# Performance work log

Hardware: AMD Instinct MI355X
Metric: run time of the kernel (lower is better)

## Reference

```python
import jax, jax.numpy as jnp
import numpy as np

DIM = 384
NUM_HEADS = 12
HEAD_DIM = DIM // NUM_HEADS  # 32
SCALE = HEAD_DIM ** -0.5
B, N = 4, 2048


def setup_inputs() -> dict:
    key = jax.random.key(0)
    k0, k1, k2, k3 = jax.random.split(key, 4)
    x = jax.random.normal(k0, (B, N, DIM), dtype=jnp.float32)
    # nn.Linear(dim, 3*dim, bias=False): y = x @ W_qkv, W_qkv is [C, 3C]
    W_qkv = jax.random.normal(k1, (DIM, 3 * DIM), dtype=jnp.float32) * (DIM ** -0.5)
    # nn.Linear(dim, dim): y = x @ W_proj + b_proj, W_proj is [C, C]
    W_proj = jax.random.normal(k2, (DIM, DIM), dtype=jnp.float32) * (DIM ** -0.5)
    b_proj = jax.random.normal(k3, (DIM,), dtype=jnp.float32) * 0.01
    return {"x": x, "W_qkv": W_qkv, "W_proj": W_proj, "b_proj": b_proj}


def reference(x, W_qkv, W_proj, b_proj):
    b, n, c = x.shape
    qkv = (x @ W_qkv).reshape(b, n, 3, NUM_HEADS, HEAD_DIM)
    qkv = jnp.transpose(qkv, (2, 0, 3, 1, 4))  # [3, B, H, N, hd]
    q, k, v = qkv[0], qkv[1], qkv[2]
    # full attention: softmax(q k^T * scale) v
    attn = jnp.einsum('bhqd,bhkd->bhqk', q, k) * SCALE  # [B,H,N,N]
    attn = jax.nn.softmax(attn, axis=-1)
    out = jnp.einsum('bhqk,bhkd->bhqd', attn, v)  # [B,H,N,hd]
    out = jnp.transpose(out, (0, 2, 1, 3)).reshape(b, n, c)
    return out @ W_proj + b_proj
```

## Files before the change

### kernel.cpp

```cpp
#include <hip/hip_runtime.h>

constexpr int BB  = 4;
constexpr int SEQ = 2048;
constexpr int CC  = 384;
constexpr int C3  = 1152;
constexpr int NH  = 12;
constexpr int HD  = 32;
constexpr float SCALE = 0.17677669529663689f;
constexpr float LOG2E = 1.4426950408889634f;
constexpr size_t KV_BYTES = (size_t)2 * BB * NH * SEQ * HD * 2;
constexpr size_t WT_BYTES = ((size_t)C3 * CC + (size_t)CC * CC) * 2;
constexpr size_t XB_BYTES = (size_t)BB * SEQ * CC * 2;

typedef __attribute__((ext_vector_type(8))) short short8_t;
typedef __attribute__((ext_vector_type(4))) float floatx4;

#if __has_builtin(__builtin_amdgcn_exp2f)
#define EXP2F __builtin_amdgcn_exp2f
#else
#define EXP2F __builtin_exp2f
#endif

__device__ __forceinline__ unsigned short f2bf(float f) {
    unsigned int u = __builtin_bit_cast(unsigned int, f);
    u += 0x7fffu + ((u >> 16) & 1u);
    return (unsigned short)(u >> 16);
}
__device__ __forceinline__ unsigned int pk_rn(float lo, float hi) {
    return __builtin_amdgcn_perm(__builtin_bit_cast(unsigned int, hi) + 0x8000u,
                                 __builtin_bit_cast(unsigned int, lo) + 0x8000u,
                                 0x07060302u);
}
__device__ __forceinline__ short8_t pack8(float4 a, float4 b) {
    uint4 u;
    u.x = pk_rn(a.x, a.y); u.y = pk_rn(a.z, a.w);
    u.z = pk_rn(b.x, b.y); u.w = pk_rn(b.z, b.w);
    return __builtin_bit_cast(short8_t, u);
}

__global__ __launch_bounds__(256) void prep_kernel(
    const float* __restrict__ x, const float* __restrict__ wqkv,
    const float* __restrict__ wproj,
    unsigned short* __restrict__ wqkvT, unsigned short* __restrict__ wprojT,
    unsigned short* __restrict__ xb)
{
    const int bid = blockIdx.x;
    if (bid >= 144) {
        const size_t base = (size_t)(bid - 144) * 2048 + threadIdx.x * 8;
        const float4 a = *(const float4*)(x + base);
        const float4 b = *(const float4*)(x + base + 4);
        uint4 u;
        u.x = pk_rn(a.x, a.y); u.y = pk_rn(a.z, a.w);
        u.z = pk_rn(b.x, b.y); u.w = pk_rn(b.z, b.w);
        *(uint4*)(xb + base) = u;
        return;
    }
    __shared__ float ls[64][68];
    const float* src; unsigned short* dst; int SN, k0, n0;
    if (bid < 108) {
        src = wqkv; dst = wqkvT; SN = C3;
        k0 = (bid / 18) * 64; n0 = (bid % 18) * 64;
    } else {
        const int b2 = bid - 108;
        src = wproj; dst = wprojT; SN = CC;
        k0 = (b2 / 6) * 64; n0 = (b2 % 6) * 64;
    }
    const int t  = threadIdx.x;
    const int rr = t >> 4, cc4 = (t & 15) * 4;
#pragma unroll
    for (int p = 0; p < 4; ++p) {
        const int row = p * 16 + rr;
        const float4 v = *(const float4*)&src[(size_t)(k0 + row) * SN + n0 + cc4];
        ls[row][cc4] = v.x; ls[row][cc4 + 1] = v.y;
        ls[row][cc4 + 2] = v.z; ls[row][cc4 + 3] = v.w;
    }
    __syncthreads();
#pragma unroll
    for (int p = 0; p < 4; ++p) {
        const int nrow = p * 16 + rr;
        uint2 u;
        u.x = pk_rn(ls[cc4][nrow],     ls[cc4 + 1][nrow]);
        u.y = pk_rn(ls[cc4 + 2][nrow], ls[cc4 + 3][nrow]);
        *(uint2*)&dst[(size_t)(n0 + nrow) * CC + k0 + cc4] = u;
    }
}

template<bool XB>
__global__ __launch_bounds__(256) void qkv_fast_t(
    const float* __restrict__ x,
    const unsigned short* __restrict__ xb,
    const unsigned short* __restrict__ wT,
    float* __restrict__ dq,
    unsigned short* __restrict__ kv)
{
    __shared__ __align__(16) unsigned short As[2][128][40];
    __shared__ __align__(16) unsigned short Bs[2][128][40];

    const int mt   = blockIdx.x & 63;
    const int nb   = blockIdx.x >> 6;
    const int tid  = threadIdx.x;
    const int wid  = tid >> 6;
    const int lane = tid & 63;
    const int quad = lane >> 4;
    const int col  = lane & 15;
    const int wr   = wid >> 1, wc = wid & 1;
    const int m0 = mt * 128, n0 = nb * 128;

    const int arow = tid >> 1;
    const int aoff = (tid & 1) * 16;

    floatx4 acc[4][4];
#pragma unroll
    for (int i = 0; i < 4; ++i)
#pragma unroll
        for (int j = 0; j < 4; ++j) acc[i][j] = (floatx4){0.f, 0.f, 0.f, 0.f};

    const float*          xrow  = x  + (size_t)(m0 + arow) * CC + aoff;
    const unsigned short* xbrow = xb + (size_t)(m0 + arow) * CC + aoff;
    const unsigned short* wrow  = wT + (size_t)(n0 + arow) * CC + aoff;

    short8_t ast0, ast1, bst0, bst1;
    if (XB) {
        ast0 = *(const short8_t*)xbrow;
        ast1 = *(const short8_t*)(xbrow + 8);
    } else {
        ast0 = pack8(*(const float4*)xrow,       *(const float4*)(xrow + 4));
        ast1 = pack8(*(const float4*)(xrow + 8), *(const float4*)(xrow + 12));
    }
    bst0 = *(const short8_t*)wrow;
    bst1 = *(const short8_t*)(wrow + 8);
    *(short8_t*)&As[0][arow][aoff]     = ast0;
    *(short8_t*)&As[0][arow][aoff + 8] = ast1;
    *(short8_t*)&Bs[0][arow][aoff]     = bst0;
    *(short8_t*)&Bs[0][arow][aoff + 8] = bst1;

    for (int it = 0; it < CC / 32; ++it) {
        const int kn = (it + 1 < CC / 32) ? (it + 1) * 32 : 0;
        if (XB) {
            ast0 = *(const short8_t*)(xbrow + kn);
            ast1 = *(const short8_t*)(xbrow + kn + 8);
        } else {
            const float* xr = xrow + kn;
            ast0 = pack8(*(const float4*)xr,       *(const float4*)(xr + 4));
            ast1 = pack8(*(const float4*)(xr + 8), *(const float4*)(xr + 12));
        }
        bst0 = *(const short8_t*)(wrow + kn);
        bst1 = *(const short8_t*)(wrow + kn + 8);

        __syncthreads();
        const int p = it & 1;
        short8_t af[4], bf[4];
#pragma unroll
        for (int i = 0; i < 4; ++i)
            af[i] = *(const short8_t*)&As[p][wr * 64 + i * 16 + col][quad * 8];
#pragma unroll
        for (int j = 0; j < 4; ++j)
            bf[j] = *(const short8_t*)&Bs[p][wc * 64 + j * 16 + col][quad * 8];
#pragma unroll
        for (int j = 0; j < 4; ++j)
#pragma unroll
            for (int i = 0; i < 4; ++i)
                acc[i][j] = __builtin_amdgcn_mfma_f32_16x16x32_bf16(af[i], bf[j], acc[i][j], 0, 0, 0);

        *(short8_t*)&As[p ^ 1][arow][aoff]     = ast0;
        *(short8_t*)&As[p ^ 1][arow][aoff + 8] = ast1;
        *(short8_t*)&Bs[p ^ 1][arow][aoff]     = bst0;
        *(short8_t*)&Bs[p ^ 1][arow][aoff + 8] = bst1;
    }

    const int t = nb / 3;
#pragma unroll
    for (int i = 0; i < 4; ++i) {
        const int mg = m0 + wr * 64 + i * 16 + quad * 4;
        if (t == 0) {
#pragma unroll
            for (int j = 0; j < 4; ++j) {
                const int n = n0 + wc * 64 + j * 16 + col;
#pragma unroll
                for (int r = 0; r < 4; ++r)
                    dq[(size_t)(mg + r) * CC + n] = acc[i][j][r];
            }
        } else if (t == 1) {
            const int b = mg >> 11, s = mg & (SEQ - 1);
#pragma unroll
            for (int j = 0; j < 4; ++j) {
                const int rem = n0 - CC + wc * 64 + j * 16 + col;
                const int h = rem >> 5, d = rem & 31;
                unsigned short* kp = kv + ((size_t)(b * NH + h) * SEQ + s) * HD + d;
#pragma unroll
                for (int r = 0; r < 4; ++r)
                    kp[(size_t)r * HD] = f2bf(acc[i][j][r]);
            }
        } else {
            const int b = mg >> 11, s = mg & (SEQ - 1);
            unsigned short* vtb = kv + (size_t)BB * NH * SEQ * HD;
#pragma unroll
            for (int j = 0; j < 4; ++j) {
                const int rem = n0 - 2 * CC + wc * 64 + j * 16 + col;
                const int h = rem >> 5, d = rem & 31;
                uint2 u;
                u.x = pk_rn(acc[i][j][0], acc[i][j][1]);
                u.y = pk_rn(acc[i][j][2], acc[i][j][3]);
                *(uint2*)&vtb[((size_t)(b * NH + h) * HD + d) * SEQ + s] = u;
            }
        }
    }
}

__global__ __launch_bounds__(256) void attn_kernel(
    const unsigned short* __restrict__ kv,
    float* qatt)
{
    const int bid  = blockIdx.x;
    const int qp   = bid / 48;
    const int bh   = bid % 48;
    const int h    = bh % NH;
    const int b    = bh / NH;
    const int w    = threadIdx.x >> 6;
    const int lane = threadIdx.x & 63;
    const int quad = lane >> 4;
    const int col  = lane & 15;
    const int tid  = threadIdx.x;

    const unsigned short* K  = kv + (size_t)bh * SEQ * HD;
    const unsigned short* VT = kv + (size_t)BB * NH * SEQ * HD + (size_t)bh * HD * SEQ;

    __shared__ __align__(16) unsigned short Kt[2][64][40];
    __shared__ __align__(16) unsigned short Vt[2][32][72];

    const int krow_s = tid >> 2, koff_s = (tid & 3) * 8;
    const int drow_s = tid >> 3, voff_s = (tid & 7) * 8;

    int qrow[2];
    short8_t qf[2];
    const float sc = SCALE * LOG2E;
#pragma unroll
    for (int t = 0; t < 2; ++t) {
        qrow[t] = b * SEQ + qp * 128 + (w + 4 * t) * 16 + col;
        const float* qpt = qatt + (size_t)qrow[t] * CC + h * HD + quad * 8;
        const float4 a0 = *(const float4*)qpt;
        const float4 a1 = *(const float4*)(qpt + 4);
        const float4 s0 = {a0.x * sc, a0.y * sc, a0.z * sc, a0.w * sc};
        const float4 s1 = {a1.x * sc, a1.y * sc, a1.z * sc, a1.w * sc};
        qf[t] = pack8(s0, s1);
    }

    short8_t ones;
#pragma unroll
    for (int e = 0; e < 8; ++e) ones[e] = (short)0x3F80;

    floatx4 o[2][2];
    floatx4 lacc[2];
#pragma unroll
    for (int t = 0; t < 2; ++t) {
        lacc[t] = (floatx4){0.f, 0.f, 0.f, 0.f};
#pragma unroll
        for (int i = 0; i < 2; ++i) o[t][i] = (floatx4){0.f, 0.f, 0.f, 0.f};
    }
    const float ci = -10.f * LOG2E;
    const floatx4 cinit = {ci, ci, ci, ci};

    short8_t kst = *(const short8_t*)(K + (size_t)krow_s * HD + koff_s);
    short8_t vst = *(const short8_t*)(VT + (size_t)drow_s * SEQ + voff_s);
    *(short8_t*)&Kt[0][krow_s][koff_s] = kst;
    *(short8_t*)&Vt[0][drow_s][voff_s] = vst;

    for (int it = 0; it < SEQ / 64; ++it) {
        const int kn = ((it + 1) * 64) & (SEQ - 1);
        kst = *(const short8_t*)(K + (size_t)(kn + krow_s) * HD + koff_s);
        vst = *(const short8_t*)(VT + (size_t)drow_s * SEQ + kn + voff_s);

        __syncthreads();
        const int p = it & 1;

#pragma unroll
        for (int c = 0; c < 2; ++c) {
            const int c32 = c * 32;
            const short8_t ka0 = *(const short8_t*)&Kt[p][c32 + col][quad * 8];
            const short8_t ka1 = *(const short8_t*)&Kt[p][c32 + 16 + col][quad * 8];
            const uint2 v0a = *(const uint2*)&Vt[p][col][c32 + quad * 4];
            const uint2 v0b = *(const uint2*)&Vt[p][col][c32 + 16 + quad * 4];
            const uint2 v1a = *(const uint2*)&Vt[p][16 + col][c32 + quad * 4];
            const uint2 v1b = *(const uint2*)&Vt[p][16 + col][c32 + 16 + quad * 4];
            const short8_t va0 = __builtin_bit_cast(short8_t, (uint4){v0a.x, v0a.y, v0b.x, v0b.y});
            const short8_t va1 = __builtin_bit_cast(short8_t, (uint4){v1a.x, v1a.y, v1b.x, v1b.y});
#pragma unroll
            for (int t = 0; t < 2; ++t) {
                const floatx4 s0 = __builtin_amdgcn_mfma_f32_16x16x32_bf16(ka0, qf[t], cinit, 0, 0, 0);
                const floatx4 s1 = __builtin_amdgcn_mfma_f32_16x16x32_bf16(ka1, qf[t], cinit, 0, 0, 0);
                const float p00 = EXP2F(s0[0]), p01 = EXP2F(s0[1]);
                const float p02 = EXP2F(s0[2]), p03 = EXP2F(s0[3]);
                const float p10 = EXP2F(s1[0]), p11 = EXP2F(s1[1]);
                const float p12 = EXP2F(s1[2]), p13 = EXP2F(s1[3]);
                const uint4 pu = {pk_rn(p00, p01), pk_rn(p02, p03),
                                  pk_rn(p10, p11), pk_rn(p12, p13)};
                const short8_t pb = __builtin_bit_cast(short8_t, pu);
                o[t][0] = __builtin_amdgcn_mfma_f32_16x16x32_bf16(va0, pb, o[t][0], 0, 0, 0);
                o[t][1] = __builtin_amdgcn_mfma_f32_16x16x32_bf16(va1, pb, o[t][1], 0, 0, 0);
                lacc[t] = __builtin_amdgcn_mfma_f32_16x16x32_bf16(ones, pb, lacc[t], 0, 0, 0);
            }
        }

        *(short8_t*)&Kt[p ^ 1][krow_s][koff_s] = kst;
        *(short8_t*)&Vt[p ^ 1][drow_s][voff_s] = vst;
    }

#pragma unroll
    for (int t = 0; t < 2; ++t) {
        const float inv = 1.f / lacc[t][0];
        float* op = qatt + (size_t)qrow[t] * CC + h * HD;
#pragma unroll
        for (int r = 0; r < 4; ++r) {
            op[quad * 4 + r]      = o[t][0][r] * inv;
            op[16 + quad * 4 + r] = o[t][1][r] * inv;
        }
    }
}

__global__ __launch_bounds__(256) void proj_fast(
    float* att,
    const unsigned short* __restrict__ wT,
    const float* __restrict__ bias)
{
    __shared__ __align__(16) unsigned short Bs[2][384][32];
    __shared__ __align__(16) unsigned short As[2][32][40];

    const int mt   = blockIdx.x;
    const int tid  = threadIdx.x;
    const int wid  = tid >> 6;
    const int lane = tid & 63;
    const int quad = lane >> 4;
    const int col  = lane & 15;
    const int m0   = mt * 32;

    const int arow = tid >> 3, akoff = (tid & 7) * 4;

    floatx4 acc[2][6];
#pragma unroll
    for (int i = 0; i < 2; ++i)
#pragma unroll
        for (int j = 0; j < 6; ++j) acc[i][j] = (floatx4){0.f, 0.f, 0.f, 0.f};

    short8_t bst[3][2];
    uint2 asr;
    {
#pragma unroll
        for (int j = 0; j < 3; ++j) {
            const int f = j * 256 + tid;
            const unsigned short* wp = wT + (size_t)(f >> 1) * CC + (f & 1) * 16;
            bst[j][0] = *(const short8_t*)wp;
            bst[j][1] = *(const short8_t*)(wp + 8);
        }
        const float4 av = *(const float4*)(att + (size_t)(m0 + arow) * CC + akoff);
        asr = (uint2){pk_rn(av.x, av.y), pk_rn(av.z, av.w)};
#pragma unroll
        for (int j = 0; j < 3; ++j) {
            const int f = j * 256 + tid;
            *(short8_t*)&Bs[0][f >> 1][(f & 1) * 16]     = bst[j][0];
            *(short8_t*)&Bs[0][f >> 1][(f & 1) * 16 + 8] = bst[j][1];
        }
        *(uint2*)&As[0][arow][akoff] = asr;
    }

    for (int it = 0; it < CC / 32; ++it) {
        const int kn = (it + 1 < CC / 32) ? (it + 1) * 32 : 0;
#pragma unroll
        for (int j = 0; j < 3; ++j) {
            const int f = j * 256 + tid;
            const unsigned short* wp = wT + (size_t)(f >> 1) * CC + kn + (f & 1) * 16;
            bst[j][0] = *(const short8_t*)wp;
            bst[j][1] = *(const short8_t*)(wp + 8);
        }
        const float4 av = *(const float4*)(att + (size_t)(m0 + arow) * CC + kn + akoff);
        asr = (uint2){pk_rn(av.x, av.y), pk_rn(av.z, av.w)};

        __syncthreads();
        const int p = it & 1;
        short8_t af[2], bf[6];
#pragma unroll
        for (int i = 0; i < 2; ++i)
            af[i] = *(const short8_t*)&As[p][i * 16 + col][quad * 8];
#pragma unroll
        for (int j = 0; j < 6; ++j)
            bf[j] = *(const short8_t*)&Bs[p][wid * 96 + j * 16 + col][quad * 8];
#pragma unroll
        for (int j = 0; j < 6; ++j)
#pragma unroll
            for (int i = 0; i < 2; ++i)
                acc[i][j] = __builtin_amdgcn_mfma_f32_16x16x32_bf16(af[i], bf[j], acc[i][j], 0, 0, 0);

#pragma unroll
        for (int j = 0; j < 3; ++j) {
            const int f = j * 256 + tid;
            *(short8_t*)&Bs[p ^ 1][f >> 1][(f & 1) * 16]     = bst[j][0];
            *(short8_t*)&Bs[p ^ 1][f >> 1][(f & 1) * 16 + 8] = bst[j][1];
        }
        *(uint2*)&As[p ^ 1][arow][akoff] = asr;
    }

    __syncthreads();
#pragma unroll
    for (int j = 0; j < 6; ++j) {
        const int n = wid * 96 + j * 16 + col;
        const float bv = bias[n];
#pragma unroll
        for (int i = 0; i < 2; ++i)
#pragma unroll
            for (int r = 0; r < 4; ++r)
                att[(size_t)(m0 + i * 16 + quad * 4 + r) * CC + n] = acc[i][j][r] + bv;
    }
}

__global__ __launch_bounds__(256) void qkv_lds(
    const float* __restrict__ x, const float* __restrict__ w,
    float* __restrict__ dq, unsigned short* __restrict__ kv)
{
    __shared__ __align__(16) unsigned short wt[128 * 40];
    const int mt = blockIdx.x & 63, nb = blockIdx.x >> 6;
    const int tid = threadIdx.x, wid = tid >> 6, lane = tid & 63;
    const int quad = lane >> 4, col = lane & 15;
    const int wr = wid >> 1, wc = wid & 1;
    const int m0 = mt * 128, n0 = nb * 128;
    const int sn = tid >> 1, skg = (tid & 1) * 4;

    floatx4 acc[4][4];
#pragma unroll
    for (int i = 0; i < 4; ++i)
#pragma unroll
        for (int j = 0; j < 4; ++j) acc[i][j] = (floatx4){0.f, 0.f, 0.f, 0.f};
    const float* xbase = x + (size_t)(m0 + wr * 64 + col) * CC;

    for (int kb = 0; kb < CC; kb += 32) {
        float wv[4][4];
#pragma unroll
        for (int s = 0; s < 4; ++s) {
            const int k = kb + (skg + s) * 4;
#pragma unroll
            for (int j = 0; j < 4; ++j) wv[s][j] = w[(size_t)(k + j) * C3 + n0 + sn];
        }
        short8_t af[4];
#pragma unroll
        for (int i = 0; i < 4; ++i) {
            const float* xr = xbase + (size_t)i * 16 * CC + kb + quad * 8;
            af[i] = pack8(*(const float4*)xr, *(const float4*)(xr + 4));
        }
        __syncthreads();
#pragma unroll
        for (int s = 0; s < 4; ++s) {
            ushort4 u;
            u.x = f2bf(wv[s][0]); u.y = f2bf(wv[s][1]);
            u.z = f2bf(wv[s][2]); u.w = f2bf(wv[s][3]);
            *(ushort4*)&wt[sn * 40 + (skg + s) * 4] = u;
        }
        __syncthreads();
#pragma unroll
        for (int j = 0; j < 4; ++j) {
            const short8_t bf = *(const short8_t*)&wt[(wc * 64 + j * 16 + col) * 40 + quad * 8];
#pragma unroll
            for (int i = 0; i < 4; ++i)
                acc[i][j] = __builtin_amdgcn_mfma_f32_16x16x32_bf16(af[i], bf, acc[i][j], 0, 0, 0);
        }
    }
    const int t = nb / 3;
#pragma unroll
    for (int i = 0; i < 4; ++i) {
        const int mg = m0 + wr * 64 + i * 16 + quad * 4;
        if (t == 0) {
#pragma unroll
            for (int j = 0; j < 4; ++j) {
                const int n = n0 + wc * 64 + j * 16 + col;
#pragma unroll
                for (int r = 0; r < 4; ++r) dq[(size_t)(mg + r) * CC + n] = acc[i][j][r];
            }
        } else if (t == 1) {
            const int b = mg >> 11, s = mg & (SEQ - 1);
#pragma unroll
            for (int j = 0; j < 4; ++j) {
                const int rem = n0 - CC + wc * 64 + j * 16 + col;
                const int h = rem >> 5, d = rem & 31;
                unsigned short* kp = kv + ((size_t)(b * NH + h) * SEQ + s) * HD + d;
#pragma unroll
                for (int r = 0; r < 4; ++r) kp[(size_t)r * HD] = f2bf(acc[i][j][r]);
            }
        } else {
            const int b = mg >> 11, s = mg & (SEQ - 1);
            unsigned short* vtb = kv + (size_t)BB * NH * SEQ * HD;
#pragma unroll
            for (int j = 0; j < 4; ++j) {
                const int rem = n0 - 2 * CC + wc * 64 + j * 16 + col;
                const int h = rem >> 5, d = rem & 31;
                uint2 u;
                u.x = pk_rn(acc[i][j][0], acc[i][j][1]);
                u.y = pk_rn(acc[i][j][2], acc[i][j][3]);
                *(uint2*)&vtb[((size_t)(b * NH + h) * HD + d) * SEQ + s] = u;
            }
        }
    }
}

__global__ __launch_bounds__(256) void proj_lds(
    float* att, const float* __restrict__ wp, const float* __restrict__ bias)
{
    __shared__ __align__(16) unsigned short wt[CC * 40];
    const int mt = blockIdx.x, tid = threadIdx.x, wid = tid >> 6, lane = tid & 63;
    const int quad = lane >> 4, col = lane & 15;
    const int m0 = mt * 16;
    floatx4 acc[6];
#pragma unroll
    for (int j = 0; j < 6; ++j) acc[j] = (floatx4){0.f, 0.f, 0.f, 0.f};
    for (int kb = 0; kb < CC; kb += 32) {
        float gv[12][4];
#pragma unroll
        for (int g = 0; g < 12; ++g) {
            const int flat = tid + g * 256, n = flat % 384, kg = flat / 384;
#pragma unroll
            for (int j = 0; j < 4; ++j) gv[g][j] = wp[(size_t)(kb + kg * 4 + j) * CC + n];
        }
        __syncthreads();
#pragma unroll
        for (int g = 0; g < 12; ++g) {
            const int flat = tid + g * 256, n = flat % 384, kg = flat / 384;
            ushort4 u;
            u.x = f2bf(gv[g][0]); u.y = f2bf(gv[g][1]);
            u.z = f2bf(gv[g][2]); u.w = f2bf(gv[g][3]);
            *(ushort4*)&wt[n * 40 + kg * 4] = u;
        }
        __syncthreads();
        const float* ap = att + (size_t)(m0 + col) * CC + kb + quad * 8;
        const short8_t af = pack8(*(const float4*)ap, *(const float4*)(ap + 4));
#pragma unroll
        for (int j = 0; j < 6; ++j) {
            const short8_t pb = *(const short8_t*)&wt[(wid * 96 + j * 16 + col) * 40 + quad * 8];
            acc[j] = __builtin_amdgcn_mfma_f32_16x16x32_bf16(af, pb, acc[j], 0, 0, 0);
        }
    }
    __syncthreads();
#pragma unroll
    for (int j = 0; j < 6; ++j) {
        const int n = wid * 96 + j * 16 + col;
        const float bv = bias[n];
#pragma unroll
        for (int r = 0; r < 4; ++r)
            att[(size_t)(m0 + quad * 4 + r) * CC + n] = acc[j][r] + bv;
    }
}

__global__ void marker_kernel(float* out, float val, int nelem) {
    int i = blockIdx.x * 256 + threadIdx.x;
    if (i < nelem) out[i] = val;
}

extern "C" void kernel_launch(void* const* d_in, const int* in_sizes, int n_in,
                              void* d_out, int out_size, void* d_ws, size_t ws_size,
                              hipStream_t stream)
{
    const float* x     = (const float*)d_in[0];
    const float* wqkv  = (const float*)d_in[1];
    const float* wproj = (const float*)d_in[2];
    const float* bproj = (const float*)d_in[3];
    float* out = (float*)d_out;
    unsigned short* kv = (unsigned short*)d_ws;

    if (ws_size < KV_BYTES) {
        const float marker = 100.f + (float)(ws_size >> 20);
        marker_kernel<<<(out_size + 255) / 256, 256, 0, stream>>>(out, marker, out_size);
        return;
    }

    unsigned short* wqkvT  = kv + (size_t)2 * BB * NH * SEQ * HD;
    unsigned short* wprojT = wqkvT + (size_t)C3 * CC;
    unsigned short* xb     = wprojT + (size_t)CC * CC;

    if (ws_size >= KV_BYTES + WT_BYTES + XB_BYTES) {
        prep_kernel<<<144 + 1536, 256, 0, stream>>>(x, wqkv, wproj, wqkvT, wprojT, xb);
        qkv_fast_t<true><<<576, 256, 0, stream>>>(x, xb, wqkvT, out, kv);
        attn_kernel<<<16 * BB * NH, 256, 0, stream>>>(kv, out);
        proj_fast<<<BB * SEQ / 32, 256, 0, stream>>>(out, wprojT, bproj);
    } else if (ws_size >= KV_BYTES + WT_BYTES) {
        prep_kernel<<<144, 256, 0, stream>>>(x, wqkv, wproj, wqkvT, wprojT, xb);
        qkv_fast_t<false><<<576, 256, 0, stream>>>(x, xb, wqkvT, out, kv);
        attn_kernel<<<16 * BB * NH, 256, 0, stream>>>(kv, out);
        proj_fast<<<BB * SEQ / 32, 256, 0, stream>>>(out, wprojT, bproj);
    } else {
        qkv_lds<<<576, 256, 0, stream>>>(x, wqkv, out, kv);
        attn_kernel<<<16 * BB * NH, 256, 0, stream>>>(kv, out);
        proj_lds<<<BB * SEQ / 16, 256, 0, stream>>>(out, wproj, bproj);
    }
}
```

Baseline: 148.3 us.

## Drop x bf16 pre-pass, shrink QKV and proj GEMM tiles for more blocks

Removes the separate x-to-bf16 conversion pass and always converts x in-register inside the QKV GEMM. The QKV GEMM N-tile shrinks from 128 to 96, giving 768 blocks instead of 576. The projection GEMM M-tile shrinks from 32 to 16 rows, doubling its grid to 512 blocks. This trades per-block reuse and extra weight reloads for better CU occupancy and one less kernel and pass over memory.

```diff
diff --git a/kernel.cpp b/kernel.cpp
--- a/kernel.cpp
+++ b/kernel.cpp
@@ -10,7 +10,6 @@
 constexpr float LOG2E = 1.4426950408889634f;
 constexpr size_t KV_BYTES = (size_t)2 * BB * NH * SEQ * HD * 2;
 constexpr size_t WT_BYTES = ((size_t)C3 * CC + (size_t)CC * CC) * 2;
-constexpr size_t XB_BYTES = (size_t)BB * SEQ * CC * 2;
 
 typedef __attribute__((ext_vector_type(8))) short short8_t;
 typedef __attribute__((ext_vector_type(4))) float floatx4;
@@ -39,22 +38,10 @@
 }
 
 __global__ __launch_bounds__(256) void prep_kernel(
-    const float* __restrict__ x, const float* __restrict__ wqkv,
-    const float* __restrict__ wproj,
-    unsigned short* __restrict__ wqkvT, unsigned short* __restrict__ wprojT,
-    unsigned short* __restrict__ xb)
+    const float* __restrict__ wqkv, const float* __restrict__ wproj,
+    unsigned short* __restrict__ wqkvT, unsigned short* __restrict__ wprojT)
 {
     const int bid = blockIdx.x;
-    if (bid >= 144) {
-        const size_t base = (size_t)(bid - 144) * 2048 + threadIdx.x * 8;
-        const float4 a = *(const float4*)(x + base);
-        const float4 b = *(const float4*)(x + base + 4);
-        uint4 u;
-        u.x = pk_rn(a.x, a.y); u.y = pk_rn(a.z, a.w);
-        u.z = pk_rn(b.x, b.y); u.w = pk_rn(b.z, b.w);
-        *(uint4*)(xb + base) = u;
-        return;
-    }
     __shared__ float ls[64][68];
     const float* src; unsigned short* dst; int SN, k0, n0;
     if (bid < 108) {
@@ -85,16 +72,14 @@
     }
 }
 
-template<bool XB>
-__global__ __launch_bounds__(256) void qkv_fast_t(
+__global__ __launch_bounds__(256) void qkv_fast(
     const float* __restrict__ x,
-    const unsigned short* __restrict__ xb,
     const unsigned short* __restrict__ wT,
     float* __restrict__ dq,
     unsigned short* __restrict__ kv)
 {
     __shared__ __align__(16) unsigned short As[2][128][40];
-    __shared__ __align__(16) unsigned short Bs[2][128][40];
+    __shared__ __align__(16) unsigned short Bs[2][96][40];
 
     const int mt   = blockIdx.x & 63;
     const int nb   = blockIdx.x >> 6;
@@ -104,78 +89,78 @@
     const int quad = lane >> 4;
     const int col  = lane & 15;
     const int wr   = wid >> 1, wc = wid & 1;
-    const int m0 = mt * 128, n0 = nb * 128;
+    const int m0 = mt * 128, n0 = nb * 96;
 
     const int arow = tid >> 1;
     const int aoff = (tid & 1) * 16;
-
-    floatx4 acc[4][4];
+    const int brow = tid >> 1;
+    const bool bact = tid < 192;
+
+    floatx4 acc[4][3];
 #pragma unroll
     for (int i = 0; i < 4; ++i)
 #pragma unroll
-        for (int j = 0; j < 4; ++j) acc[i][j] = (floatx4){0.f, 0.f, 0.f, 0.f};
-
-    const float*          xrow  = x  + (size_t)(m0 + arow) * CC + aoff;
-    const unsigned short* xbrow = xb + (size_t)(m0 + arow) * CC + aoff;
-    const unsigned short* wrow  = wT + (size_t)(n0 + arow) * CC + aoff;
+        for (int j = 0; j < 3; ++j) acc[i][j] = (floatx4){0.f, 0.f, 0.f, 0.f};
+
+    const float*          xrow = x  + (size_t)(m0 + arow) * CC + aoff;
+    const unsigned short* wrow = wT + (size_t)(n0 + brow) * CC + aoff;
 
     short8_t ast0, ast1, bst0, bst1;
-    if (XB) {
-        ast0 = *(const short8_t*)xbrow;
-        ast1 = *(const short8_t*)(xbrow + 8);
-    } else {
-        ast0 = pack8(*(const float4*)xrow,       *(const float4*)(xrow + 4));
-        ast1 = pack8(*(const float4*)(xrow + 8), *(const float4*)(xrow + 12));
-    }
-    bst0 = *(const short8_t*)wrow;
-    bst1 = *(const short8_t*)(wrow + 8);
+    ast0 = pack8(*(const float4*)xrow,        *(const float4*)(xrow + 4));
+    ast1 = pack8(*(const float4*)(xrow + 8),  *(const float4*)(xrow + 12));
+    if (bact) {
+        bst0 = *(const short8_t*)wrow;
+        bst1 = *(const short8_t*)(wrow + 8);
+    }
     *(short8_t*)&As[0][arow][aoff]     = ast0;
     *(short8_t*)&As[0][arow][aoff + 8] = ast1;
-    *(short8_t*)&Bs[0][arow][aoff]     = bst0;
-    *(short8_t*)&Bs[0][arow][aoff + 8] = bst1;
+    if (bact) {
+        *(short8_t*)&Bs[0][brow][aoff]     = bst0;
+        *(short8_t*)&Bs[0][brow][aoff + 8] = bst1;
+    }
 
     for (int it = 0; it < CC / 32; ++it) {
         const int kn = (it + 1 < CC / 32) ? (it + 1) * 32 : 0;
-        if (XB) {
-            ast0 = *(const short8_t*)(xbrow + kn);
-            ast1 = *(const short8_t*)(xbrow + kn + 8);
-        } else {
-            const float* xr = xrow + kn;
-            ast0 = pack8(*(const float4*)xr,       *(const float4*)(xr + 4));
-            ast1 = pack8(*(const float4*)(xr + 8), *(const float4*)(xr + 12));
-        }
-        bst0 = *(const short8_t*)(wrow + kn);
-        bst1 = *(const short8_t*)(wrow + kn + 8);
+        const float* xr = xrow + kn;
+        ast0 = pack8(*(const float4*)xr,       *(const float4*)(xr + 4));
+        ast1 = pack8(*(const float4*)(xr + 8), *(const float4*)(xr + 12));
+        if (bact) {
+            bst0 = *(const short8_t*)(wrow + kn);
+            bst1 = *(const short8_t*)(wrow + kn + 8);
+        }
 
         __syncthreads();
         const int p = it & 1;
-        short8_t af[4], bf[4];
+        short8_t af[4], bf[3];
 #pragma unroll
         for (int i = 0; i < 4; ++i)
             af[i] = *(const short8_t*)&As[p][wr * 64 + i * 16 + col][quad * 8];
 #pragma unroll
-        for (int j = 0; j < 4; ++j)
-            bf[j] = *(const short8_t*)&Bs[p][wc * 64 + j * 16 + col][quad * 8];
-#pragma unroll
-        for (int j = 0; j < 4; ++j)
+        for (int j = 0; j < 3; ++j)
+            bf[j] = *(const short8_t*)&Bs[p][wc * 48 + j * 16 + col][quad * 8];
+#pragma unroll
+        for (int j = 0; j < 3; ++j)
 #pragma unroll
             for (int i = 0; i < 4; ++i)
                 acc[i][j] = __builtin_amdgcn_mfma_f32_16x16x32_bf16(af[i], bf[j], acc[i][j], 0, 0, 0);
 
         *(short8_t*)&As[p ^ 1][arow][aoff]     = ast0;
         *(short8_t*)&As[p ^ 1][arow][aoff + 8] = ast1;
-        *(short8_t*)&Bs[p ^ 1][arow][aoff]     = bst0;
-        *(short8_t*)&Bs[p ^ 1][arow][aoff + 8] = bst1;
-    }
-
-    const int t = nb / 3;
+        if (bact) {
+            *(short8_t*)&Bs[p ^ 1][brow][aoff]     = bst0;
+            *(short8_t*)&Bs[p ^ 1][brow][aoff + 8] = bst1;
+        }
+    }
+
+    const int t    = nb >> 2;
+    const int remb = (nb & 3) * 96;
 #pragma unroll
     for (int i = 0; i < 4; ++i) {
         const int mg = m0 + wr * 64 + i * 16 + quad * 4;
         if (t == 0) {
 #pragma unroll
-            for (int j = 0; j < 4; ++j) {
-                const int n = n0 + wc * 64 + j * 16 + col;
+            for (int j = 0; j < 3; ++j) {
+                const int n = n0 + wc * 48 + j * 16 + col;
 #pragma unroll
                 for (int r = 0; r < 4; ++r)
                     dq[(size_t)(mg + r) * CC + n] = acc[i][j][r];
@@ -183,8 +168,8 @@
         } else if (t == 1) {
             const int b = mg >> 11, s = mg & (SEQ - 1);
 #pragma unroll
-            for (int j = 0; j < 4; ++j) {
-                const int rem = n0 - CC + wc * 64 + j * 16 + col;
+            for (int j = 0; j < 3; ++j) {
+                const int rem = remb + wc * 48 + j * 16 + col;
                 const int h = rem >> 5, d = rem & 31;
                 unsigned short* kp = kv + ((size_t)(b * NH + h) * SEQ + s) * HD + d;
 #pragma unroll
@@ -195,8 +180,8 @@
             const int b = mg >> 11, s = mg & (SEQ - 1);
             unsigned short* vtb = kv + (size_t)BB * NH * SEQ * HD;
 #pragma unroll
-            for (int j = 0; j < 4; ++j) {
-                const int rem = n0 - 2 * CC + wc * 64 + j * 16 + col;
+            for (int j = 0; j < 3; ++j) {
+                const int rem = remb + wc * 48 + j * 16 + col;
                 const int h = rem >> 5, d = rem & 31;
                 uint2 u;
                 u.x = pk_rn(acc[i][j][0], acc[i][j][1]);
@@ -323,7 +308,7 @@
     const float* __restrict__ bias)
 {
     __shared__ __align__(16) unsigned short Bs[2][384][32];
-    __shared__ __align__(16) unsigned short As[2][32][40];
+    __shared__ __align__(16) unsigned short As[2][16][40];
 
     const int mt   = blockIdx.x;
     const int tid  = threadIdx.x;
@@ -331,18 +316,16 @@
     const int lane = tid & 63;
     const int quad = lane >> 4;
     const int col  = lane & 15;
-    const int m0   = mt * 32;
-
-    const int arow = tid >> 3, akoff = (tid & 7) * 4;
-
-    floatx4 acc[2][6];
-#pragma unroll
-    for (int i = 0; i < 2; ++i)
-#pragma unroll
-        for (int j = 0; j < 6; ++j) acc[i][j] = (floatx4){0.f, 0.f, 0.f, 0.f};
+    const int m0   = mt * 16;
+
+    const int arow = tid >> 4, akoff = (tid & 15) * 2;
+
+    floatx4 acc[6];
+#pragma unroll
+    for (int j = 0; j < 6; ++j) acc[j] = (floatx4){0.f, 0.f, 0.f, 0.f};
 
     short8_t bst[3][2];
-    uint2 asr;
+    unsigned int asr;
     {
 #pragma unroll
         for (int j = 0; j < 3; ++j) {
@@ -351,15 +334,15 @@
             bst[j][0] = *(const short8_t*)wp;
             bst[j][1] = *(const short8_t*)(wp + 8);
         }
-        const float4 av = *(const float4*)(att + (size_t)(m0 + arow) * CC + akoff);
-        asr = (uint2){pk_rn(av.x, av.y), pk_rn(av.z, av.w)};
+        const float2 av = *(const float2*)(att + (size_t)(m0 + arow) * CC + akoff);
+        asr = pk_rn(av.x, av.y);
 #pragma unroll
         for (int j = 0; j < 3; ++j) {
             const int f = j * 256 + tid;
             *(short8_t*)&Bs[0][f >> 1][(f & 1) * 16]     = bst[j][0];
             *(short8_t*)&Bs[0][f >> 1][(f & 1) * 16 + 8] = bst[j][1];
         }
-        *(uint2*)&As[0][arow][akoff] = asr;
+        *(unsigned int*)&As[0][arow][akoff] = asr;
     }
 
     for (int it = 0; it < CC / 32; ++it) {
@@ -371,23 +354,19 @@
             bst[j][0] = *(const short8_t*)wp;
             bst[j][1] = *(const short8_t*)(wp + 8);
         }
-        const float4 av = *(const float4*)(att + (size_t)(m0 + arow) * CC + kn + akoff);
-        asr = (uint2){pk_rn(av.x, av.y), pk_rn(av.z, av.w)};
+        const float2 av = *(const float2*)(att + (size_t)(m0 + arow) * CC + kn + akoff);
+        asr = pk_rn(av.x, av.y);
 
         __syncthreads();
         const int p = it & 1;
-        short8_t af[2], bf[6];
-#pragma unroll
-        for (int i = 0; i < 2; ++i)
-            af[i] = *(const short8_t*)&As[p][i * 16 + col][quad * 8];
+        const short8_t af = *(const short8_t*)&As[p][col][quad * 8];
+        short8_t bf[6];
 #pragma unroll
         for (int j = 0; j < 6; ++j)
             bf[j] = *(const short8_t*)&Bs[p][wid * 96 + j * 16 + col][quad * 8];
 #pragma unroll
         for (int j = 0; j < 6; ++j)
-#pragma unroll
-            for (int i = 0; i < 2; ++i)
-                acc[i][j] = __builtin_amdgcn_mfma_f32_16x16x32_bf16(af[i], bf[j], acc[i][j], 0, 0, 0);
+            acc[j] = __builtin_amdgcn_mfma_f32_16x16x32_bf16(af, bf[j], acc[j], 0, 0, 0);
 
 #pragma unroll
         for (int j = 0; j < 3; ++j) {
@@ -395,7 +374,7 @@
             *(short8_t*)&Bs[p ^ 1][f >> 1][(f & 1) * 16]     = bst[j][0];
             *(short8_t*)&Bs[p ^ 1][f >> 1][(f & 1) * 16 + 8] = bst[j][1];
         }
-        *(uint2*)&As[p ^ 1][arow][akoff] = asr;
+        *(unsigned int*)&As[p ^ 1][arow][akoff] = asr;
     }
 
     __syncthreads();
@@ -404,10 +383,8 @@
         const int n = wid * 96 + j * 16 + col;
         const float bv = bias[n];
 #pragma unroll
-        for (int i = 0; i < 2; ++i)
-#pragma unroll
-            for (int r = 0; r < 4; ++r)
-                att[(size_t)(m0 + i * 16 + quad * 4 + r) * CC + n] = acc[i][j][r] + bv;
+        for (int r = 0; r < 4; ++r)
+            att[(size_t)(m0 + quad * 4 + r) * CC + n] = acc[j][r] + bv;
     }
 }
 
@@ -569,18 +546,12 @@
 
     unsigned short* wqkvT  = kv + (size_t)2 * BB * NH * SEQ * HD;
     unsigned short* wprojT = wqkvT + (size_t)C3 * CC;
-    unsigned short* xb     = wprojT + (size_t)CC * CC;
-
-    if (ws_size >= KV_BYTES + WT_BYTES + XB_BYTES) {
-        prep_kernel<<<144 + 1536, 256, 0, stream>>>(x, wqkv, wproj, wqkvT, wprojT, xb);
-        qkv_fast_t<true><<<576, 256, 0, stream>>>(x, xb, wqkvT, out, kv);
+
+    if (ws_size >= KV_BYTES + WT_BYTES) {
+        prep_kernel<<<144, 256, 0, stream>>>(wqkv, wproj, wqkvT, wprojT);
+        qkv_fast<<<12 * 64, 256, 0, stream>>>(x, wqkvT, out, kv);
         attn_kernel<<<16 * BB * NH, 256, 0, stream>>>(kv, out);
-        proj_fast<<<BB * SEQ / 32, 256, 0, stream>>>(out, wprojT, bproj);
-    } else if (ws_size >= KV_BYTES + WT_BYTES) {
-        prep_kernel<<<144, 256, 0, stream>>>(x, wqkv, wproj, wqkvT, wprojT, xb);
-        qkv_fast_t<false><<<576, 256, 0, stream>>>(x, xb, wqkvT, out, kv);
-        attn_kernel<<<16 * BB * NH, 256, 0, stream>>>(kv, out);
-        proj_fast<<<BB * SEQ / 32, 256, 0, stream>>>(out, wprojT, bproj);
+        proj_fast<<<BB * SEQ / 16, 256, 0, stream>>>(out, wprojT, bproj);
     } else {
         qkv_lds<<<576, 256, 0, stream>>>(x, wqkv, out, kv);
         attn_kernel<<<16 * BB * NH, 256, 0, stream>>>(kv, out);
```

Result: slower. 152.4 us (+2.8%).

## Drop x bf16 pre-conversion and double attention key tile to 128

Applied to the files above, without the earlier changes.

Removes the separate x-to-bf16 conversion blocks in the prep kernel, so the QKV GEMM always reads fp32 x and packs it to bf16 on the fly. The attention kernel now stages 128 keys per iteration instead of 64, with each thread loading two 16-byte chunks of K and V, which halves the number of loop iterations and barriers. The cost is larger LDS use per block, which may reduce occupancy, and the QKV GEMM now reads twice the activation bytes.

```diff
diff --git a/kernel.cpp b/kernel.cpp
--- a/kernel.cpp
+++ b/kernel.cpp
@@ -10,7 +10,6 @@
 constexpr float LOG2E = 1.4426950408889634f;
 constexpr size_t KV_BYTES = (size_t)2 * BB * NH * SEQ * HD * 2;
 constexpr size_t WT_BYTES = ((size_t)C3 * CC + (size_t)CC * CC) * 2;
-constexpr size_t XB_BYTES = (size_t)BB * SEQ * CC * 2;
 
 typedef __attribute__((ext_vector_type(8))) short short8_t;
 typedef __attribute__((ext_vector_type(4))) float floatx4;
@@ -39,22 +38,10 @@
 }
 
 __global__ __launch_bounds__(256) void prep_kernel(
-    const float* __restrict__ x, const float* __restrict__ wqkv,
-    const float* __restrict__ wproj,
-    unsigned short* __restrict__ wqkvT, unsigned short* __restrict__ wprojT,
-    unsigned short* __restrict__ xb)
+    const float* __restrict__ wqkv, const float* __restrict__ wproj,
+    unsigned short* __restrict__ wqkvT, unsigned short* __restrict__ wprojT)
 {
     const int bid = blockIdx.x;
-    if (bid >= 144) {
-        const size_t base = (size_t)(bid - 144) * 2048 + threadIdx.x * 8;
-        const float4 a = *(const float4*)(x + base);
-        const float4 b = *(const float4*)(x + base + 4);
-        uint4 u;
-        u.x = pk_rn(a.x, a.y); u.y = pk_rn(a.z, a.w);
-        u.z = pk_rn(b.x, b.y); u.w = pk_rn(b.z, b.w);
-        *(uint4*)(xb + base) = u;
-        return;
-    }
     __shared__ float ls[64][68];
     const float* src; unsigned short* dst; int SN, k0, n0;
     if (bid < 108) {
@@ -85,10 +72,8 @@
     }
 }
 
-template<bool XB>
-__global__ __launch_bounds__(256) void qkv_fast_t(
+__global__ __launch_bounds__(256) void qkv_fast(
     const float* __restrict__ x,
-    const unsigned short* __restrict__ xb,
     const unsigned short* __restrict__ wT,
     float* __restrict__ dq,
     unsigned short* __restrict__ kv)
@@ -115,18 +100,12 @@
 #pragma unroll
         for (int j = 0; j < 4; ++j) acc[i][j] = (floatx4){0.f, 0.f, 0.f, 0.f};
 
-    const float*          xrow  = x  + (size_t)(m0 + arow) * CC + aoff;
-    const unsigned short* xbrow = xb + (size_t)(m0 + arow) * CC + aoff;
-    const unsigned short* wrow  = wT + (size_t)(n0 + arow) * CC + aoff;
+    const float*          xrow = x  + (size_t)(m0 + arow) * CC + aoff;
+    const unsigned short* wrow = wT + (size_t)(n0 + arow) * CC + aoff;
 
     short8_t ast0, ast1, bst0, bst1;
-    if (XB) {
-        ast0 = *(const short8_t*)xbrow;
-        ast1 = *(const short8_t*)(xbrow + 8);
-    } else {
-        ast0 = pack8(*(const float4*)xrow,       *(const float4*)(xrow + 4));
-        ast1 = pack8(*(const float4*)(xrow + 8), *(const float4*)(xrow + 12));
-    }
+    ast0 = pack8(*(const float4*)xrow,        *(const float4*)(xrow + 4));
+    ast1 = pack8(*(const float4*)(xrow + 8),  *(const float4*)(xrow + 12));
     bst0 = *(const short8_t*)wrow;
     bst1 = *(const short8_t*)(wrow + 8);
     *(short8_t*)&As[0][arow][aoff]     = ast0;
@@ -136,14 +115,9 @@
 
     for (int it = 0; it < CC / 32; ++it) {
         const int kn = (it + 1 < CC / 32) ? (it + 1) * 32 : 0;
-        if (XB) {
-            ast0 = *(const short8_t*)(xbrow + kn);
-            ast1 = *(const short8_t*)(xbrow + kn + 8);
-        } else {
-            const float* xr = xrow + kn;
-            ast0 = pack8(*(const float4*)xr,       *(const float4*)(xr + 4));
-            ast1 = pack8(*(const float4*)(xr + 8), *(const float4*)(xr + 12));
-        }
+        const float* xr = xrow + kn;
+        ast0 = pack8(*(const float4*)xr,       *(const float4*)(xr + 4));
+        ast1 = pack8(*(const float4*)(xr + 8), *(const float4*)(xr + 12));
         bst0 = *(const short8_t*)(wrow + kn);
         bst1 = *(const short8_t*)(wrow + kn + 8);
 
@@ -225,11 +199,11 @@
     const unsigned short* K  = kv + (size_t)bh * SEQ * HD;
     const unsigned short* VT = kv + (size_t)BB * NH * SEQ * HD + (size_t)bh * HD * SEQ;
 
-    __shared__ __align__(16) unsigned short Kt[2][64][40];
-    __shared__ __align__(16) unsigned short Vt[2][32][72];
-
-    const int krow_s = tid >> 2, koff_s = (tid & 3) * 8;
-    const int drow_s = tid >> 3, voff_s = (tid & 7) * 8;
+    __shared__ __align__(16) unsigned short Kt[2][128][40];
+    __shared__ __align__(16) unsigned short Vt[2][32][136];
+
+    const int krow_s = tid >> 1, koff_s = (tid & 1) * 16;
+    const int drow_s = tid >> 3, voff_s = (tid & 7) * 16;
 
     int qrow[2];
     short8_t qf[2];
@@ -260,30 +234,36 @@
     const float ci = -10.f * LOG2E;
     const floatx4 cinit = {ci, ci, ci, ci};
 
-    short8_t kst = *(const short8_t*)(K + (size_t)krow_s * HD + koff_s);
-    short8_t vst = *(const short8_t*)(VT + (size_t)drow_s * SEQ + voff_s);
-    *(short8_t*)&Kt[0][krow_s][koff_s] = kst;
-    *(short8_t*)&Vt[0][drow_s][voff_s] = vst;
-
-    for (int it = 0; it < SEQ / 64; ++it) {
-        const int kn = ((it + 1) * 64) & (SEQ - 1);
-        kst = *(const short8_t*)(K + (size_t)(kn + krow_s) * HD + koff_s);
-        vst = *(const short8_t*)(VT + (size_t)drow_s * SEQ + kn + voff_s);
+    short8_t k0a = *(const short8_t*)(K + (size_t)krow_s * HD + koff_s);
+    short8_t k0b = *(const short8_t*)(K + (size_t)krow_s * HD + koff_s + 8);
+    short8_t v0a = *(const short8_t*)(VT + (size_t)drow_s * SEQ + voff_s);
+    short8_t v0b = *(const short8_t*)(VT + (size_t)drow_s * SEQ + voff_s + 8);
+    *(short8_t*)&Kt[0][krow_s][koff_s]     = k0a;
+    *(short8_t*)&Kt[0][krow_s][koff_s + 8] = k0b;
+    *(short8_t*)&Vt[0][drow_s][voff_s]     = v0a;
+    *(short8_t*)&Vt[0][drow_s][voff_s + 8] = v0b;
+
+    for (int it = 0; it < SEQ / 128; ++it) {
+        const int kn = ((it + 1) * 128) & (SEQ - 1);
+        k0a = *(const short8_t*)(K + (size_t)(kn + krow_s) * HD + koff_s);
+        k0b = *(const short8_t*)(K + (size_t)(kn + krow_s) * HD + koff_s + 8);
+        v0a = *(const short8_t*)(VT + (size_t)drow_s * SEQ + kn + voff_s);
+        v0b = *(const short8_t*)(VT + (size_t)drow_s * SEQ + kn + voff_s + 8);
 
         __syncthreads();
         const int p = it & 1;
 
 #pragma unroll
-        for (int c = 0; c < 2; ++c) {
+        for (int c = 0; c < 4; ++c) {
             const int c32 = c * 32;
             const short8_t ka0 = *(const short8_t*)&Kt[p][c32 + col][quad * 8];
             const short8_t ka1 = *(const short8_t*)&Kt[p][c32 + 16 + col][quad * 8];
-            const uint2 v0a = *(const uint2*)&Vt[p][col][c32 + quad * 4];
-            const uint2 v0b = *(const uint2*)&Vt[p][col][c32 + 16 + quad * 4];
-            const uint2 v1a = *(const uint2*)&Vt[p][16 + col][c32 + quad * 4];
-            const uint2 v1b = *(const uint2*)&Vt[p][16 + col][c32 + 16 + quad * 4];
-            const short8_t va0 = __builtin_bit_cast(short8_t, (uint4){v0a.x, v0a.y, v0b.x, v0b.y});
-            const short8_t va1 = __builtin_bit_cast(short8_t, (uint4){v1a.x, v1a.y, v1b.x, v1b.y});
+            const uint2 w0a = *(const uint2*)&Vt[p][col][c32 + quad * 4];
+            const uint2 w0b = *(const uint2*)&Vt[p][col][c32 + 16 + quad * 4];
+            const uint2 w1a = *(const uint2*)&Vt[p][16 + col][c32 + quad * 4];
+            const uint2 w1b = *(const uint2*)&Vt[p][16 + col][c32 + 16 + quad * 4];
+            const short8_t va0 = __builtin_bit_cast(short8_t, (uint4){w0a.x, w0a.y, w0b.x, w0b.y});
+            const short8_t va1 = __builtin_bit_cast(short8_t, (uint4){w1a.x, w1a.y, w1b.x, w1b.y});
 #pragma unroll
             for (int t = 0; t < 2; ++t) {
                 const floatx4 s0 = __builtin_amdgcn_mfma_f32_16x16x32_bf16(ka0, qf[t], cinit, 0, 0, 0);
@@ -301,8 +281,10 @@
             }
         }
 
-        *(short8_t*)&Kt[p ^ 1][krow_s][koff_s] = kst;
-        *(short8_t*)&Vt[p ^ 1][drow_s][voff_s] = vst;
+        *(short8_t*)&Kt[p ^ 1][krow_s][koff_s]     = k0a;
+        *(short8_t*)&Kt[p ^ 1][krow_s][koff_s + 8] = k0b;
+        *(short8_t*)&Vt[p ^ 1][drow_s][voff_s]     = v0a;
+        *(short8_t*)&Vt[p ^ 1][drow_s][voff_s + 8] = v0b;
     }
 
 #pragma unroll
@@ -569,16 +551,10 @@
 
     unsigned short* wqkvT  = kv + (size_t)2 * BB * NH * SEQ * HD;
     unsigned short* wprojT = wqkvT + (size_t)C3 * CC;
-    unsigned short* xb     = wprojT + (size_t)CC * CC;
-
-    if (ws_size >= KV_BYTES + WT_BYTES + XB_BYTES) {
-        prep_kernel<<<144 + 1536, 256, 0, stream>>>(x, wqkv, wproj, wqkvT, wprojT, xb);
-        qkv_fast_t<true><<<576, 256, 0, stream>>>(x, xb, wqkvT, out, kv);
-        attn_kernel<<<16 * BB * NH, 256, 0, stream>>>(kv, out);
-        proj_fast<<<BB * SEQ / 32, 256, 0, stream>>>(out, wprojT, bproj);
-    } else if (ws_size >= KV_BYTES + WT_BYTES) {
-        prep_kernel<<<144, 256, 0, stream>>>(x, wqkv, wproj, wqkvT, wprojT, xb);
-        qkv_fast_t<false><<<576, 256, 0, stream>>>(x, xb, wqkvT, out, kv);
+
+    if (ws_size >= KV_BYTES + WT_BYTES) {
+        prep_kernel<<<144, 256, 0, stream>>>(wqkv, wproj, wqkvT, wprojT);
+        qkv_fast<<<576, 256, 0, stream>>>(x, wqkvT, out, kv);
         attn_kernel<<<16 * BB * NH, 256, 0, stream>>>(kv, out);
         proj_fast<<<BB * SEQ / 32, 256, 0, stream>>>(out, wprojT, bproj);
     } else {
```

Result: slower. 153.3 us (+3.4%).
